# Performance work log

Hardware: AMD Instinct MI355X
Metric: run time of the kernel (lower is better)

## Reference

```python
import jax, jax.numpy as jnp
import numpy as np

EPS = 1e-5

def _bn(x):
    # training-mode batchnorm (batch stats), gamma=1 beta=0 per the module's init
    ax = tuple(range(x.ndim - 1))
    m = x.mean(ax, keepdims=True)
    v = x.var(ax, keepdims=True)
    return (x - m) * jax.lax.rsqrt(v + EPS)

def _mlp(x, weights):
    # shared 1x1-conv MLP: pointwise linear -> BN -> ReLU
    for W in weights:
        x = jax.nn.relu(_bn(jnp.einsum('...c,oc->...o', x, W)))
    return x

def _fps_single(xyz, npoint):
    # farthest point sampling, xyz [N,3] -> [npoint] int32 indices
    N = xyz.shape[0]
    def step(carry, _):
        dists, far = carry
        d = jnp.sum((xyz - xyz[far]) ** 2, -1)
        dists = jnp.minimum(dists, d)
        return (dists, jnp.argmax(dists).astype(jnp.int32)), far
    init = (jnp.full((N,), 1e10, xyz.dtype), jnp.int32(0))
    _, idx = jax.lax.scan(step, init, None, length=npoint)
    return idx

def _ball_query(new_xyz, xyz, radius, nsample):
    # first nsample points (in original order) within radius of each center
    d2 = jnp.sum((new_xyz[:, :, None, :] - xyz[:, None, :, :]) ** 2, -1)  # [B,S,N]
    N = xyz.shape[1]
    rank = jnp.where(d2 < radius * radius, jnp.arange(N, dtype=jnp.int32), jnp.int32(N))
    vals, _ = jax.lax.top_k(-rank, nsample)
    idx = -vals
    idx = jnp.where(idx == N, idx[..., :1], idx)  # pad with first valid (center itself)
    return idx

def _gather(pts, idx):
    # pts [B,N,C], idx [B,S,ns] -> [B,S,ns,C]
    B, S, ns = idx.shape
    return jnp.take_along_axis(pts, idx.reshape(B, S * ns, 1), axis=1).reshape(B, S, ns, pts.shape[-1])

def _sa(xyz, feats, npoint, radius, nsample, weights):
    fps_idx = jax.vmap(_fps_single, in_axes=(0, None))(xyz, npoint)
    new_xyz = jnp.take_along_axis(xyz, fps_idx[:, :, None], axis=1)  # [B,S,3]
    idx = _ball_query(new_xyz, xyz, radius, nsample)
    g_xyz = (_gather(xyz, idx) - new_xyz[:, :, None, :]) / radius  # normalize_xyz
    x = g_xyz if feats is None else jnp.concatenate([g_xyz, _gather(feats, idx)], -1)
    x = _mlp(x, weights)
    return new_xyz, x.max(axis=2), fps_idx  # maxpool over nsample

def _forward(obj_cloud, gripper_cloud, sa1_w0, sa1_w1, sa1_w2, sa2_w0, sa2_w1, sa2_w2,
             sa3_w0, sa3_w1, sa3_w2, ge_w0, ge_w1, ge_w2,
             head_w0, head_b0, head_w1, head_b1, head_w2, head_b2):
    # gripper encoder: pointwise conv1d MLP + global maxpool
    g = _mlp(gripper_cloud, [ge_w0, ge_w1, ge_w2])      # [B,G,128]
    gripper_feature = g.max(axis=1)                      # [B,128]
    # backbone
    xyz1, f1, _ = _sa(obj_cloud, None, 512, 0.2, 32, [sa1_w0, sa1_w1, sa1_w2])
    xyz2, f2, _ = _sa(xyz1, f1, 128, 0.4, 64, [sa2_w0, sa2_w1, sa2_w2])
    # sa3: group_all (use_xyz, no centering/normalization)
    x = jnp.concatenate([xyz2, f2], -1)[:, None]         # [B,1,128,259]
    x = _mlp(x, [sa3_w0, sa3_w1, sa3_w2])
    obj_feature = x.max(axis=2)[:, 0]                    # [B,1024]
    comb = jnp.concatenate([gripper_feature, obj_feature], -1)  # [B,1152]
    h = _bn(comb)
    h = jax.nn.relu(_bn(h @ head_w0.T + head_b0))
    h = jax.nn.relu(_bn(h @ head_w1.T + head_b1))
    return jax.nn.relu(h @ head_w2.T + head_b2)          # [B,1]

def setup_inputs() -> dict:
    key = jax.random.key(0)
    ks = jax.random.split(key, 24)
    def w(k, o, i):
        return (jax.random.normal(k, (o, i), jnp.float32) * 0.05)
    inp = {
        'obj_cloud': jax.random.uniform(ks[0], (8, 20000, 3), jnp.float32),
        'gripper_cloud': jax.random.uniform(ks[1], (8, 512, 3), jnp.float32),
        'sa1_w0': w(ks[2], 64, 3),   'sa1_w1': w(ks[3], 64, 64),   'sa1_w2': w(ks[4], 128, 64),
        'sa2_w0': w(ks[5], 128, 131),'sa2_w1': w(ks[6], 128, 128), 'sa2_w2': w(ks[7], 256, 128),
        'sa3_w0': w(ks[8], 256, 259),'sa3_w1': w(ks[9], 512, 256), 'sa3_w2': w(ks[10], 1024, 512),
        'ge_w0': w(ks[11], 64, 3),   'ge_w1': w(ks[12], 128, 64),  'ge_w2': w(ks[13], 128, 128),
        'head_w0': w(ks[14], 512, 1152), 'head_b0': jnp.zeros((512,), jnp.float32),
        'head_w1': w(ks[15], 256, 512),  'head_b1': jnp.zeros((256,), jnp.float32),
        'head_w2': w(ks[16], 1, 256),    'head_b2': jnp.zeros((1,), jnp.float32),
    }
    return inp

def reference(obj_cloud, gripper_cloud, sa1_w0, sa1_w1, sa1_w2, sa2_w0, sa2_w1, sa2_w2,
              sa3_w0, sa3_w1, sa3_w2, ge_w0, ge_w1, ge_w2,
              head_w0, head_b0, head_w1, head_b1, head_w2, head_b2):
    return _forward(obj_cloud, gripper_cloud, sa1_w0, sa1_w1, sa1_w2, sa2_w0, sa2_w1, sa2_w2,
                    sa3_w0, sa3_w1, sa3_w2, ge_w0, ge_w1, ge_w2,
                    head_w0, head_b0, head_w1, head_b1, head_w2, head_b2)
```

## Files before the change

### kernel.cpp

```cpp
#include <hip/hip_runtime.h>
#include <cstddef>
#include <cstdint>

#define EPS_BN 1e-5f
#define NBINS 4
#define NEG_INF (-__builtin_inff())

template <bool FUSE_IN, bool FUSE_MAX>
__global__ __launch_bounds__(256) void gemm_xwt(const float* __restrict__ X,
                                                const float* __restrict__ Wm,
                                                float* __restrict__ Y,
                                                int R, int Cin, int Cout,
                                                const float* __restrict__ st_in, int Rin,
                                                float* __restrict__ st_out,
                                                float* __restrict__ pooled, int ns) {
  __shared__ __align__(16) float Xs[16][132];
  __shared__ __align__(16) float Ws[16][132];
  __shared__ float sMean[512], sScale[512];
  const int t  = threadIdx.x;
  const int r0 = blockIdx.x << 7;
  const int n0 = blockIdx.y << 7;
  const int tx = t & 15;
  const int ty = t >> 4;

  if constexpr (FUSE_IN) {
    const float inv = 1.f / (float)Rin;
    for (int k = t; k < Cin; k += 256) {
      float s = 0.f, q = 0.f;
#pragma unroll
      for (int bn = 0; bn < NBINS; ++bn) {
        s += st_in[bn * 2 * Cin + k];
        q += st_in[bn * 2 * Cin + Cin + k];
      }
      const float m  = s * inv;
      const float vr = fmaf(-m, m, q * inv);
      sMean[k]  = m;
      sScale[k] = rsqrtf(vr + EPS_BN);
    }
    __syncthreads();
  }

  float acc[8][8] = {};
  const int rStage = t >> 1;
  const int kBase  = (t & 1) << 3;
  const int nr     = n0 + rStage;

  for (int k0 = 0; k0 < Cin; k0 += 16) {
    const float* xrow = X  + (size_t)(r0 + rStage) * Cin + k0 + kBase;
    const float* wrow = Wm + (size_t)nr * Cin + k0 + kBase;
    if (((Cin & 3) == 0) && (k0 + 16 <= Cin)) {
      float4 xa = *(const float4*)(xrow);
      float4 xb = *(const float4*)(xrow + 4);
      if constexpr (FUSE_IN) {
        const int kb = k0 + kBase;
        xa.x = fmaxf(0.f, (xa.x - sMean[kb + 0]) * sScale[kb + 0]);
        xa.y = fmaxf(0.f, (xa.y - sMean[kb + 1]) * sScale[kb + 1]);
        xa.z = fmaxf(0.f, (xa.z - sMean[kb + 2]) * sScale[kb + 2]);
        xa.w = fmaxf(0.f, (xa.w - sMean[kb + 3]) * sScale[kb + 3]);
        xb.x = fmaxf(0.f, (xb.x - sMean[kb + 4]) * sScale[kb + 4]);
        xb.y = fmaxf(0.f, (xb.y - sMean[kb + 5]) * sScale[kb + 5]);
        xb.z = fmaxf(0.f, (xb.z - sMean[kb + 6]) * sScale[kb + 6]);
        xb.w = fmaxf(0.f, (xb.w - sMean[kb + 7]) * sScale[kb + 7]);
      }
      Xs[kBase + 0][rStage] = xa.x; Xs[kBase + 1][rStage] = xa.y;
      Xs[kBase + 2][rStage] = xa.z; Xs[kBase + 3][rStage] = xa.w;
      Xs[kBase + 4][rStage] = xb.x; Xs[kBase + 5][rStage] = xb.y;
      Xs[kBase + 6][rStage] = xb.z; Xs[kBase + 7][rStage] = xb.w;
      float4 wa = {0, 0, 0, 0}, wb = {0, 0, 0, 0};
      if (nr < Cout) { wa = *(const float4*)(wrow); wb = *(const float4*)(wrow + 4); }
      Ws[kBase + 0][rStage] = wa.x; Ws[kBase + 1][rStage] = wa.y;
      Ws[kBase + 2][rStage] = wa.z; Ws[kBase + 3][rStage] = wa.w;
      Ws[kBase + 4][rStage] = wb.x; Ws[kBase + 5][rStage] = wb.y;
      Ws[kBase + 6][rStage] = wb.z; Ws[kBase + 7][rStage] = wb.w;
    } else {
#pragma unroll
      for (int u = 0; u < 8; ++u) {
        const int k = k0 + kBase + u;
        float xe = 0.f, we = 0.f;
        if (k < Cin) {
          xe = xrow[u];
          if constexpr (FUSE_IN) xe = fmaxf(0.f, (xe - sMean[k]) * sScale[k]);
          if (nr < Cout) we = wrow[u];
        }
        Xs[kBase + u][rStage] = xe;
        Ws[kBase + u][rStage] = we;
      }
    }
    __syncthreads();
#pragma unroll
    for (int kk = 0; kk < 16; ++kk) {
      const float4 a0 = *(const float4*)(&Xs[kk][ty << 2]);
      const float4 a1 = *(const float4*)(&Xs[kk][64 + (ty << 2)]);
      const float4 b0 = *(const float4*)(&Ws[kk][tx << 2]);
      const float4 b1 = *(const float4*)(&Ws[kk][64 + (tx << 2)]);
      const float av[8] = {a0.x, a0.y, a0.z, a0.w, a1.x, a1.y, a1.z, a1.w};
      const float bw[8] = {b0.x, b0.y, b0.z, b0.w, b1.x, b1.y, b1.z, b1.w};
#pragma unroll
      for (int i = 0; i < 8; ++i)
#pragma unroll
        for (int j = 0; j < 8; ++j) acc[i][j] = fmaf(av[i], bw[j], acc[i][j]);
    }
    __syncthreads();
  }
  if constexpr (!FUSE_MAX) {
#pragma unroll
    for (int h = 0; h < 2; ++h)
#pragma unroll
      for (int i = 0; i < 4; ++i) {
        const int r = r0 + h * 64 + (ty << 2) + i;
        float* yr = Y + (size_t)r * Cout;
#pragma unroll
        for (int g = 0; g < 2; ++g) {
          const int n = n0 + g * 64 + (tx << 2);
          if (n < Cout) {
            float4 o = {acc[h * 4 + i][g * 4 + 0], acc[h * 4 + i][g * 4 + 1],
                        acc[h * 4 + i][g * 4 + 2], acc[h * 4 + i][g * 4 + 3]};
            *(float4*)(yr + n) = o;
          }
        }
      }
  }
#pragma unroll
  for (int g = 0; g < 2; ++g)
#pragma unroll
    for (int j = 0; j < 4; ++j) {
      float s = 0.f, q = 0.f;
#pragma unroll
      for (int rh = 0; rh < 8; ++rh) {
        const float v = acc[rh][g * 4 + j];
        s += v;
        q = fmaf(v, v, q);
      }
      Xs[ty][g * 64 + (tx << 2) + j] = s;
      Ws[ty][g * 64 + (tx << 2) + j] = q;
    }
  __syncthreads();
  if (t < 128) {
    const int n = n0 + t;
    if (n < Cout) {
      float s = 0.f, q = 0.f;
#pragma unroll
      for (int w = 0; w < 16; ++w) { s += Xs[w][t]; q += Ws[w][t]; }
      float* dst = st_out + (blockIdx.x & (NBINS - 1)) * 2 * Cout;
      atomicAdd(dst + n, s);
      atomicAdd(dst + Cout + n, q);
    }
  }
  if constexpr (FUSE_MAX) {
    __syncthreads();
    float mxAll = NEG_INF;
#pragma unroll
    for (int h = 0; h < 2; ++h) {
#pragma unroll
      for (int g2 = 0; g2 < 2; ++g2)
#pragma unroll
        for (int j = 0; j < 4; ++j) {
          float mx = acc[h * 4 + 0][g2 * 4 + j];
          mx = fmaxf(mx, acc[h * 4 + 1][g2 * 4 + j]);
          mx = fmaxf(mx, acc[h * 4 + 2][g2 * 4 + j]);
          mx = fmaxf(mx, acc[h * 4 + 3][g2 * 4 + j]);
          Xs[ty][g2 * 64 + (tx << 2) + j] = mx;
        }
      __syncthreads();
      if (t < 128) {
        const int n = n0 + t;
        if (n < Cout) {
          if (ns <= 64) {
            const int tpg = ns >> 2;
            const int gph = 64 / ns;
            for (int gq = 0; gq < gph; ++gq) {
              float mx = NEG_INF;
              for (int w = gq * tpg; w < gq * tpg + tpg; ++w) mx = fmaxf(mx, Xs[w][t]);
              const int g = (r0 + h * 64) / ns + gq;
              pooled[(size_t)g * Cout + n] = mx;
            }
          } else {
            float mx = NEG_INF;
            for (int w = 0; w < 16; ++w) mx = fmaxf(mx, Xs[w][t]);
            mxAll = fmaxf(mxAll, mx);
          }
        }
      }
      __syncthreads();
    }
    if (ns > 64 && t < 128) {
      const int n = n0 + t;
      if (n < Cout) pooled[(size_t)(r0 >> 7) * Cout + n] = mxAll;
    }
  }
}

__global__ void bn_apply_pooled(const float* __restrict__ P, const float* __restrict__ st,
                                float* __restrict__ o, int G, int C, int Rtrue) {
  const int i = blockIdx.x * 256 + threadIdx.x;
  if (i >= G * C) return;
  const int c = i % C;
  float s = 0.f, q = 0.f;
#pragma unroll
  for (int bn = 0; bn < NBINS; ++bn) {
    s += st[bn * 2 * C + c];
    q += st[bn * 2 * C + C + c];
  }
  const float inv = 1.f / (float)Rtrue;
  const float m  = s * inv;
  const float vr = fmaf(-m, m, q * inv);
  const float sc = rsqrtf(vr + EPS_BN);
  o[i] = fmaxf(0.f, (P[i] - m) * sc);
}

__global__ void bn_apply_relu_maxpool(const float* __restrict__ Y,
                                      const float* __restrict__ st,
                                      float* __restrict__ o, int G, int ns, int C) {
  const int i = blockIdx.x * 256 + threadIdx.x;
  if (i >= G * C) return;
  const int c = i % C;
  const int g = i / C;
  float s = 0.f, q = 0.f;
#pragma unroll
  for (int bn = 0; bn < NBINS; ++bn) {
    s += st[bn * 2 * C + c];
    q += st[bn * 2 * C + C + c];
  }
  const int R = G * ns;
  const float inv = 1.f / (float)R;
  const float m  = s * inv;
  const float vr = fmaf(-m, m, q * inv);
  const float sc = rsqrtf(vr + EPS_BN);
  const float* p = Y + (size_t)g * ns * C + c;
  float mx = NEG_INF;
  for (int k = 0; k < ns; ++k) mx = fmaxf(mx, p[(size_t)k * C]);
  o[i] = fmaxf(0.f, (mx - m) * sc);
}

#define FPS_N 20000
#define FPS_S 512
#define FPS_NC 6
#define FPS_NCELL 216

__global__ __launch_bounds__(1024)
void fps_sa1_kernel(const float* __restrict__ xyz, float* __restrict__ new_xyz,
                    float* __restrict__ scratch) {
  const int b    = blockIdx.x;
  const int tid  = threadIdx.x;
  const int lane = tid & 63;
  const int wave = tid >> 6;
  const float* p = xyz + (size_t)b * FPS_N * 3;
  float* gxs = scratch + (size_t)b * FPS_N * 4;
  float* gys = gxs + FPS_N;
  float* gzs = gys + FPS_N;
  int*   gis = (int*)(gzs + FPS_N);

  __shared__ float ddS[FPS_N];
  __shared__ int   cStart[FPS_NCELL + 1];
  __shared__ int   cCnt[FPS_NCELL];
  __shared__ int   cFill[FPS_NCELL];
  __shared__ float ubV[FPS_NCELL];
  __shared__ int   ubI[FPS_NCELL];
  __shared__ float ubX[FPS_NCELL], ubY[FPS_NCELL], ubZ[FPS_NCELL];
  __shared__ float bc[3];
  __shared__ float wred[16 * 6];
  __shared__ float sC[10];

  float mnx = 1e30f, mny = 1e30f, mnz = 1e30f;
  float mxx = -1e30f, mxy = -1e30f, mxz = -1e30f;
  for (int i = tid; i < FPS_N; i += 1024) {
    const float x = p[i * 3 + 0], y = p[i * 3 + 1], z = p[i * 3 + 2];
    mnx = fminf(mnx, x); mny = fminf(mny, y); mnz = fminf(mnz, z);
    mxx = fmaxf(mxx, x); mxy = fmaxf(mxy, y); mxz = fmaxf(mxz, z);
  }
#pragma unroll
  for (int m = 1; m < 64; m <<= 1) {
    mnx = fminf(mnx, __shfl_xor(mnx, m, 64));
    mny = fminf(mny, __shfl_xor(mny, m, 64));
    mnz = fminf(mnz, __shfl_xor(mnz, m, 64));
    mxx = fmaxf(mxx, __shfl_xor(mxx, m, 64));
    mxy = fmaxf(mxy, __shfl_xor(mxy, m, 64));
    mxz = fmaxf(mxz, __shfl_xor(mxz, m, 64));
  }
  if (lane == 0) {
    wred[wave * 6 + 0] = mnx; wred[wave * 6 + 1] = mny; wred[wave * 6 + 2] = mnz;
    wred[wave * 6 + 3] = mxx; wred[wave * 6 + 4] = mxy; wred[wave * 6 + 5] = mxz;
  }
  if (tid < FPS_NCELL) { cCnt[tid] = 0; cFill[tid] = 0; }
  __syncthreads();
  if (tid == 0) {
    float a0 = wred[0], a1 = wred[1], a2 = wred[2];
    float a3 = wred[3], a4 = wred[4], a5 = wred[5];
    for (int w = 1; w < 16; ++w) {
      a0 = fminf(a0, wred[w * 6 + 0]); a1 = fminf(a1, wred[w * 6 + 1]);
      a2 = fminf(a2, wred[w * 6 + 2]); a3 = fmaxf(a3, wred[w * 6 + 3]);
      a4 = fmaxf(a4, wred[w * 6 + 4]); a5 = fmaxf(a5, wred[w * 6 + 5]);
    }
    const float ex = fmaxf(a3 - a0, 1e-9f);
    const float ey = fmaxf(a4 - a1, 1e-9f);
    const float ez = fmaxf(a5 - a2, 1e-9f);
    sC[0] = a0; sC[1] = a1; sC[2] = a2;
    sC[3] = (float)FPS_NC / ex; sC[4] = (float)FPS_NC / ey; sC[5] = (float)FPS_NC / ez;
    sC[6] = ex / (float)FPS_NC; sC[7] = ey / (float)FPS_NC; sC[8] = ez / (float)FPS_NC;
    sC[9] = fmaxf(ex, fmaxf(ey, ez)) * 1e-5f;
  }
  __syncthreads();
  const float bx0 = sC[0], by0 = sC[1], bz0 = sC[2];
  const float scx = sC[3], scy = sC[4], scz = sC[5];
  const float hx  = sC[6], hy  = sC[7], hz  = sC[8], ec = sC[9];

  for (int i = tid; i < FPS_N; i += 1024) {
    const float x = p[i * 3 + 0], y = p[i * 3 + 1], z = p[i * 3 + 2];
    const int cx = min(FPS_NC - 1, max(0, (int)((x - bx0) * scx)));
    const int cy = min(FPS_NC - 1, max(0, (int)((y - by0) * scy)));
    const int cz = min(FPS_NC - 1, max(0, (int)((z - bz0) * scz)));
    atomicAdd(&cCnt[(cx * FPS_NC + cy) * FPS_NC + cz], 1);
  }
  __syncthreads();
  if (tid == 0) {
    int acc = 0;
    for (int k = 0; k < FPS_NCELL; ++k) { cStart[k] = acc; acc += cCnt[k]; }
    cStart[FPS_NCELL] = acc;
  }
  __syncthreads();
  for (int i = tid; i < FPS_N; i += 1024) {
    const float x = p[i * 3 + 0], y = p[i * 3 + 1], z = p[i * 3 + 2];
    const int cx = min(FPS_NC - 1, max(0, (int)((x - bx0) * scx)));
    const int cy = min(FPS_NC - 1, max(0, (int)((y - by0) * scy)));
    const int cz = min(FPS_NC - 1, max(0, (int)((z - bz0) * scz)));
    const int cid = (cx * FPS_NC + cy) * FPS_NC + cz;
    const int pos = cStart[cid] + atomicAdd(&cFill[cid], 1);
    gxs[pos] = x; gys[pos] = y; gzs[pos] = z; gis[pos] = i;
  }
  for (int j = tid; j < FPS_N; j += 1024) ddS[j] = 1e10f;
  if (tid < FPS_NCELL) {
    ubV[tid] = (cCnt[tid] > 0) ? 1e10f : NEG_INF;
    ubI[tid] = 0x7fffffff;
  }
  __syncthreads();

  float fx = p[0], fy = p[1], fz = p[2];
  if (tid == 0) {
    float* o = new_xyz + (size_t)b * FPS_S * 3;
    o[0] = fx; o[1] = fy; o[2] = fz;
  }

  for (int s = 1; s < FPS_S; ++s) {
    const int cq = wave + (lane << 4);
    bool aff = false;
    if (cq < FPS_NCELL) {
      const int cx  = cq / (FPS_NC * FPS_NC);
      const int rem = cq - cx * (FPS_NC * FPS_NC);
      const int cy  = rem / FPS_NC;
      const int cz  = rem - cy * FPS_NC;
      const float lox = fmaf((float)cx, hx, bx0) - ec;
      const float hix = fmaf((float)(cx + 1), hx, bx0) + ec;
      const float loy = fmaf((float)cy, hy, by0) - ec;
      const float hiy = fmaf((float)(cy + 1), hy, by0) + ec;
      const float loz = fmaf((float)cz, hz, bz0) - ec;
      const float hiz = fmaf((float)(cz + 1), hz, bz0) + ec;
      const float dx = fmaxf(0.f, fmaxf(lox - fx, fx - hix));
      const float dy = fmaxf(0.f, fmaxf(loy - fy, fy - hiy));
      const float dz = fmaxf(0.f, fmaxf(loz - fz, fz - hiz));
      const float dmin = dx * dx + dy * dy + dz * dz;
      aff = (dmin * 0.99999f < ubV[cq]);
    }
    unsigned long long am = __ballot(aff);
    while (am) {
      const int l = __ffsll((long long)am) - 1;
      am &= am - 1;
      const int cc  = wave + (l << 4);
      const int st0 = cStart[cc];
      const int cn  = cStart[cc + 1] - st0;
      float bv = NEG_INF; int bi = 0x7fffffff;
      float bx = 0.f, by = 0.f, bz = 0.f;
      for (int j = lane; j < cn; j += 64) {
        const int g = st0 + j;
        const float qx = gxs[g], qy = gys[g], qz = gzs[g];
        const float dx = qx - fx, dy = qy - fy, dz = qz - fz;
        const float d  = __fadd_rn(__fadd_rn(__fmul_rn(dx, dx), __fmul_rn(dy, dy)),
                                   __fmul_rn(dz, dz));
        const float nd = fminf(ddS[g], d);
        ddS[g] = nd;
        const int gi = gis[g];
        if (nd > bv || (nd == bv && gi < bi)) { bv = nd; bi = gi; bx = qx; by = qy; bz = qz; }
      }
      float v = bv; int i0 = bi;
#pragma unroll
      for (int m = 1; m < 64; m <<= 1) {
        const float ov = __shfl_xor(v, m, 64);
        const int   oi = __shfl_xor(i0, m, 64);
        if (ov > v || (ov == v && oi < i0)) { v = ov; i0 = oi; }
      }
      if (v == bv && i0 == bi && bi != 0x7fffffff) {
        ubV[cc] = v; ubI[cc] = i0; ubX[cc] = bx; ubY[cc] = by; ubZ[cc] = bz;
      }
    }
    __syncthreads();
    if (tid < 64) {
      float v = NEG_INF; int i0 = 0x7fffffff; int c0 = 0;
#pragma unroll
      for (int q = 0; q < 4; ++q) {
        const int k = lane + (q << 6);
        if (k < FPS_NCELL) {
          const float ov = ubV[k]; const int oi = ubI[k];
          if (ov > v || (ov == v && oi < i0)) { v = ov; i0 = oi; c0 = k; }
        }
      }
#pragma unroll
      for (int m = 1; m < 64; m <<= 1) {
        const float ov = __shfl_xor(v, m, 64);
        const int   oi = __shfl_xor(i0, m, 64);
        const int   oc = __shfl_xor(c0, m, 64);
        if (ov > v || (ov == v && oi < i0)) { v = ov; i0 = oi; c0 = oc; }
      }
      if (lane == 0) {
        const float wx = ubX[c0], wy = ubY[c0], wz = ubZ[c0];
        bc[0] = wx; bc[1] = wy; bc[2] = wz;
        float* o = new_xyz + ((size_t)b * FPS_S + s) * 3;
        o[0] = wx; o[1] = wy; o[2] = wz;
      }
    }
    __syncthreads();
    fx = bc[0]; fy = bc[1]; fz = bc[2];
  }
}

template <int N, int NP, int THREADS, int NPT>
__global__ __launch_bounds__(THREADS)
void fps2_kernel(const float* __restrict__ xyz, float* __restrict__ new_xyz) {
  constexpr int NW = THREADS / 64;
  const int b    = blockIdx.x;
  const int tid  = threadIdx.x;
  const int lane = tid & 63;
  const int wave = tid >> 6;
  const float* p = xyz + (size_t)b * N * 3;
  float px[NPT], py[NPT], pz[NPT], dd[NPT];
#pragma unroll
  for (int j = 0; j < NPT; ++j) {
    const int i = tid + j * THREADS;
    if (i < N) {
      px[j] = p[i * 3 + 0];
      py[j] = p[i * 3 + 1];
      pz[j] = p[i * 3 + 2];
      dd[j] = 1e10f;
    } else {
      px[j] = 0.f; py[j] = 0.f; pz[j] = 0.f;
      dd[j] = NEG_INF;
    }
  }
  __shared__ float sv[NW], sx[NW], sy[NW], sz[NW];
  __shared__ int   si[NW];
  __shared__ float bc[3];
  float fx = p[0], fy = p[1], fz = p[2];
  if (tid == 0) {
    float* o = new_xyz + (size_t)b * NP * 3;
    o[0] = fx; o[1] = fy; o[2] = fz;
  }
  for (int s = 1; s < NP; ++s) {
    float bv = NEG_INF;
    int   bi = 0x7fffffff;
    float bx = 0.f, by = 0.f, bz = 0.f;
#pragma unroll
    for (int j = 0; j < NPT; ++j) {
      const float dx = px[j] - fx;
      const float dy = py[j] - fy;
      const float dz = pz[j] - fz;
      const float d  = __fadd_rn(__fadd_rn(__fmul_rn(dx, dx), __fmul_rn(dy, dy)),
                                 __fmul_rn(dz, dz));
      const float nd = fminf(dd[j], d);
      dd[j] = nd;
      if (nd > bv) { bv = nd; bi = tid + j * THREADS; bx = px[j]; by = py[j]; bz = pz[j]; }
    }
    float v = bv;
    int   i0 = bi;
#pragma unroll
    for (int m = 1; m < 64; m <<= 1) {
      const float ov = __shfl_xor(v, m, 64);
      const int   oi = __shfl_xor(i0, m, 64);
      if (ov > v || (ov == v && oi < i0)) { v = ov; i0 = oi; }
    }
    if (i0 == bi) {
      sv[wave] = bv; si[wave] = bi; sx[wave] = bx; sy[wave] = by; sz[wave] = bz;
    }
    __syncthreads();
    if (tid < 64) {
      const float lv = (lane < NW) ? sv[lane] : NEG_INF;
      const int   li = (lane < NW) ? si[lane] : 0x7fffffff;
      float v2 = lv;
      int   i2 = li;
#pragma unroll
      for (int m = 1; m < NW; m <<= 1) {
        const float ov = __shfl_xor(v2, m, 64);
        const int   oi = __shfl_xor(i2, m, 64);
        if (ov > v2 || (ov == v2 && oi < i2)) { v2 = ov; i2 = oi; }
      }
      if (lane < NW && li == i2) {
        const float wx = sx[lane], wy = sy[lane], wz = sz[lane];
        bc[0] = wx; bc[1] = wy; bc[2] = wz;
        float* o = new_xyz + ((size_t)b * NP + s) * 3;
        o[0] = wx; o[1] = wy; o[2] = wz;
      }
    }
    __syncthreads();
    fx = bc[0]; fy = bc[1]; fz = bc[2];
  }
}

template <int N, int NS>
__global__ __launch_bounds__(256)
void ballquery_wave_kernel(const float* __restrict__ centers,
                           const float* __restrict__ pts,
                           int* __restrict__ idx, int BS, int S, float r2) {
  const int w    = (blockIdx.x * 256 + threadIdx.x) >> 6;
  const int lane = threadIdx.x & 63;
  if (w >= BS) return;
  const int b = w / S;
  const float cx = centers[w * 3 + 0];
  const float cy = centers[w * 3 + 1];
  const float cz = centers[w * 3 + 2];
  const float* p = pts + (size_t)b * N * 3;
  int* o = idx + (size_t)w * NS;
  int total = 0;
  int first = -1;
  for (int i0 = 0; i0 < N && total < NS; i0 += 64) {
    const int i = i0 + lane;
    bool pred = false;
    if (i < N) {
      const float dx = cx - p[i * 3 + 0];
      const float dy = cy - p[i * 3 + 1];
      const float dz = cz - p[i * 3 + 2];
      const float d2 = __fadd_rn(__fadd_rn(__fmul_rn(dx, dx), __fmul_rn(dy, dy)),
                                 __fmul_rn(dz, dz));
      pred = (d2 < r2);
    }
    const unsigned long long mask = __ballot(pred);
    if (mask) {
      const unsigned long long below = (lane == 0) ? 0ull : (mask << (64 - lane));
      const int before = __popcll(below);
      if (pred && (total + before) < NS) o[total + before] = i;
      if (first < 0) first = i0 + (__ffsll((long long)mask) - 1);
      total += __popcll(mask);
    }
  }
  if (lane >= total && lane < NS) o[lane] = first;
}

__global__ void group1_kernel(const float* __restrict__ xyz, const float* __restrict__ ctr,
                              const int* __restrict__ idx, float* __restrict__ X1) {
  const int t = blockIdx.x * 256 + threadIdx.x;
  if (t >= 8 * 512 * 32) return;
  const int g = t >> 5;
  const int b = g >> 9;
  const int i = idx[t];
  const float* p = xyz + ((size_t)b * 20000 + i) * 3;
  const float* c = ctr + (size_t)g * 3;
  X1[t * 3 + 0] = (p[0] - c[0]) / 0.2f;
  X1[t * 3 + 1] = (p[1] - c[1]) / 0.2f;
  X1[t * 3 + 2] = (p[2] - c[2]) / 0.2f;
}

__global__ void group2_kernel(const float* __restrict__ xyz1,
                              const float* __restrict__ xyz2,
                              const float* __restrict__ f1,
                              const int* __restrict__ idx2,
                              float* __restrict__ X2) {
  const int t = blockIdx.x * 256 + threadIdx.x;
  if (t >= 65536 * 131) return;
  const int r = t / 131;
  const int c = t - r * 131;
  const int g = r >> 6;
  const int b = g >> 7;
  const int i = idx2[r];
  float v;
  if (c < 3) {
    v = (xyz1[((size_t)b * 512 + i) * 3 + c] - xyz2[(size_t)g * 3 + c]) / 0.4f;
  } else {
    v = f1[((size_t)b * 512 + i) * 128 + (c - 3)];
  }
  X2[t] = v;
}

__global__ void build_x3_kernel(const float* __restrict__ xyz2, const float* __restrict__ f2,
                                float* __restrict__ X3) {
  const int t = blockIdx.x * 256 + threadIdx.x;
  if (t >= 1024 * 259) return;
  const int r = t / 259;
  const int c = t - r * 259;
  X3[t] = (c < 3) ? xyz2[r * 3 + c] : f2[(size_t)r * 256 + (c - 3)];
}

__global__ __launch_bounds__(512) void head_kernel(
    const float* __restrict__ gfeat, const float* __restrict__ objf,
    const float* __restrict__ w0, const float* __restrict__ b0,
    const float* __restrict__ w1, const float* __restrict__ b1,
    const float* __restrict__ w2, const float* __restrict__ b2,
    float* __restrict__ out) {
  __shared__ __align__(16) float comb[8 * 1152];
  __shared__ __align__(16) float h1[8 * 512];
  __shared__ __align__(16) float h2[8 * 256];
  const int tid = threadIdx.x;
  for (int i = tid; i < 8 * 1152; i += 512) {
    const int b = i / 1152, c = i - b * 1152;
    comb[i] = (c < 128) ? gfeat[b * 128 + c] : objf[b * 1024 + (c - 128)];
  }
  __syncthreads();
  for (int c = tid; c < 1152; c += 512) {
    float s = 0.f;
#pragma unroll
    for (int b = 0; b < 8; ++b) s += comb[b * 1152 + c];
    const float m = s * 0.125f;
    float v = 0.f;
#pragma unroll
    for (int b = 0; b < 8; ++b) { const float d = comb[b * 1152 + c] - m; v = fmaf(d, d, v); }
    const float sc = rsqrtf(v * 0.125f + EPS_BN);
#pragma unroll
    for (int b = 0; b < 8; ++b) comb[b * 1152 + c] = (comb[b * 1152 + c] - m) * sc;
  }
  __syncthreads();
  {
    float a[8];
#pragma unroll
    for (int b = 0; b < 8; ++b) a[b] = b0[tid];
    const float* wr = w0 + (size_t)tid * 1152;
    for (int ci = 0; ci < 1152; ci += 4) {
      const float4 wv = *(const float4*)(wr + ci);
#pragma unroll
      for (int b = 0; b < 8; ++b) {
        const float4 xv = *(const float4*)(&comb[b * 1152 + ci]);
        a[b] = fmaf(xv.x, wv.x, a[b]);
        a[b] = fmaf(xv.y, wv.y, a[b]);
        a[b] = fmaf(xv.z, wv.z, a[b]);
        a[b] = fmaf(xv.w, wv.w, a[b]);
      }
    }
    float s = 0.f;
#pragma unroll
    for (int b = 0; b < 8; ++b) s += a[b];
    const float m = s * 0.125f;
    float v = 0.f;
#pragma unroll
    for (int b = 0; b < 8; ++b) { const float d = a[b] - m; v = fmaf(d, d, v); }
    const float sc = rsqrtf(v * 0.125f + EPS_BN);
#pragma unroll
    for (int b = 0; b < 8; ++b) h1[b * 512 + tid] = fmaxf(0.f, (a[b] - m) * sc);
  }
  __syncthreads();
  if (tid < 256) {
    float a[8];
#pragma unroll
    for (int b = 0; b < 8; ++b) a[b] = b1[tid];
    const float* wr = w1 + (size_t)tid * 512;
    for (int ci = 0; ci < 512; ci += 4) {
      const float4 wv = *(const float4*)(wr + ci);
#pragma unroll
      for (int b = 0; b < 8; ++b) {
        const float4 xv = *(const float4*)(&h1[b * 512 + ci]);
        a[b] = fmaf(xv.x, wv.x, a[b]);
        a[b] = fmaf(xv.y, wv.y, a[b]);
        a[b] = fmaf(xv.z, wv.z, a[b]);
        a[b] = fmaf(xv.w, wv.w, a[b]);
      }
    }
    float s = 0.f;
#pragma unroll
    for (int b = 0; b < 8; ++b) s += a[b];
    const float m = s * 0.125f;
    float v = 0.f;
#pragma unroll
    for (int b = 0; b < 8; ++b) { const float d = a[b] - m; v = fmaf(d, d, v); }
    const float sc = rsqrtf(v * 0.125f + EPS_BN);
#pragma unroll
    for (int b = 0; b < 8; ++b) h2[b * 256 + tid] = fmaxf(0.f, (a[b] - m) * sc);
  }
  __syncthreads();
  if (tid < 8) {
    float s = b2[0];
    for (int ci = 0; ci < 256; ++ci) s = fmaf(h2[tid * 256 + ci], w2[ci], s);
    out[tid] = fmaxf(0.f, s);
  }
}

extern "C" void kernel_launch(void* const* d_in, const int* in_sizes, int n_in,
                              void* d_out, int out_size, void* d_ws, size_t ws_size,
                              hipStream_t stream) {
  (void)in_sizes; (void)n_in; (void)out_size; (void)ws_size;
  const float* obj  = (const float*)d_in[0];
  const float* grip = (const float*)d_in[1];
  const float* s1w0 = (const float*)d_in[2];
  const float* s1w1 = (const float*)d_in[3];
  const float* s1w2 = (const float*)d_in[4];
  const float* s2w0 = (const float*)d_in[5];
  const float* s2w1 = (const float*)d_in[6];
  const float* s2w2 = (const float*)d_in[7];
  const float* s3w0 = (const float*)d_in[8];
  const float* s3w1 = (const float*)d_in[9];
  const float* s3w2 = (const float*)d_in[10];
  const float* gw0  = (const float*)d_in[11];
  const float* gw1  = (const float*)d_in[12];
  const float* gw2  = (const float*)d_in[13];
  const float* hw0  = (const float*)d_in[14];
  const float* hb0  = (const float*)d_in[15];
  const float* hw1  = (const float*)d_in[16];
  const float* hb1  = (const float*)d_in[17];
  const float* hw2  = (const float*)d_in[18];
  const float* hb2  = (const float*)d_in[19];
  float* out = (float*)d_out;

  float* wsf   = (float*)d_ws;
  float* stats = wsf;
  float* xyz1  = wsf + 23040;
  float* xyz2  = wsf + 35328;
  float* gfeat = wsf + 38400;
  float* objf  = wsf + 39424;
  float* f1    = wsf + 47616;
  float* f2    = wsf + 571904;
  float* x3    = wsf + 834048;
  int*   idx1  = (int*)(wsf + 1099264);
  int*   idx2  = (int*)(wsf + 1230336);
  float* bufP  = wsf + 1295872;
  float* bufQ  = wsf + 18073088;
  float* fpsScratch = bufP + 8388608;

  static const int st_off[12] = {0, 512, 1536, 2560, 3072, 3584,
                                 4608, 5632, 6656, 8704, 10752, 14848};
  auto st = [&](int li) { return stats + st_off[li]; };

  hipMemsetAsync(stats, 0, 23040 * sizeof(float), stream);

  auto gemm0 = [&](const float* X, const float* Wm, float* Y, int R, int Cin, int Cout,
                   int lo) {
    dim3 g((R + 127) / 128, (Cout + 127) / 128);
    gemm_xwt<false, false><<<g, 256, 0, stream>>>(X, Wm, Y, R, Cin, Cout, nullptr, 0,
                                                  st(lo), nullptr, 0);
  };
  auto gemmf = [&](const float* X, const float* Wm, float* Y, int R, int Cin, int Cout,
                   int li, int lo) {
    dim3 g((R + 127) / 128, (Cout + 127) / 128);
    gemm_xwt<true, false><<<g, 256, 0, stream>>>(X, Wm, Y, R, Cin, Cout, st(li), R,
                                                 st(lo), nullptr, 0);
  };
  auto gemmfM = [&](const float* X, const float* Wm, float* pooled, int R, int Cin,
                    int Cout, int li, int lo, int ns) {
    dim3 g((R + 127) / 128, (Cout + 127) / 128);
    gemm_xwt<true, true><<<g, 256, 0, stream>>>(X, Wm, nullptr, R, Cin, Cout, st(li), R,
                                                st(lo), pooled, ns);
  };
  auto applymax_k = [&](const float* Y, int li, int G, int ns, int C, float* o) {
    const int n = G * C;
    bn_apply_relu_maxpool<<<(n + 255) / 256, 256, 0, stream>>>(Y, st(li), o, G, ns, C);
  };
  auto applypool_k = [&](const float* P, int li, int G, int C, int Rtrue, float* o) {
    const int n = G * C;
    bn_apply_pooled<<<(n + 255) / 256, 256, 0, stream>>>(P, st(li), o, G, C, Rtrue);
  };

  fps_sa1_kernel<<<8, 1024, 0, stream>>>(obj, xyz1, fpsScratch);

  float* gY1 = bufP;
  float* gY2 = bufP + 262144;
  float* gY3 = bufP + 786432;
  gemm0(grip, gw0, gY1, 4096, 3, 64, 0);
  gemmf(gY1, gw1, gY2, 4096, 64, 128, 0, 1);
  gemmf(gY2, gw2, gY3, 4096, 128, 128, 1, 2);
  applymax_k(gY3, 2, 8, 512, 128, gfeat);

  ballquery_wave_kernel<20000, 32><<<1024, 256, 0, stream>>>(xyz1, obj, idx1, 4096, 512, 0.04f);
  float* X1 = bufQ;
  group1_kernel<<<512, 256, 0, stream>>>(obj, xyz1, idx1, X1);
  gemm0(X1, s1w0, bufP, 131072, 3, 64, 3);
  gemmf(bufP, s1w1, bufQ, 131072, 64, 64, 3, 4);
  gemmfM(bufQ, s1w2, bufP, 131072, 64, 128, 4, 5, 32);
  applypool_k(bufP, 5, 4096, 128, 131072, f1);

  fps2_kernel<512, 128, 256, 2><<<8, 256, 0, stream>>>(xyz1, xyz2);
  ballquery_wave_kernel<512, 64><<<256, 256, 0, stream>>>(xyz2, xyz1, idx2, 1024, 128, 0.16f);
  float* X2 = bufQ;
  group2_kernel<<<(65536 * 131 + 255) / 256, 256, 0, stream>>>(xyz1, xyz2, f1, idx2, X2);
  gemm0(X2, s2w0, bufP, 65536, 131, 128, 6);
  gemmf(bufP, s2w1, bufQ, 65536, 128, 128, 6, 7);
  gemmfM(bufQ, s2w2, bufP, 65536, 128, 256, 7, 8, 64);
  applypool_k(bufP, 8, 1024, 256, 65536, f2);

  build_x3_kernel<<<(1024 * 259 + 255) / 256, 256, 0, stream>>>(xyz2, f2, x3);
  float* Y3a = bufQ;
  float* Y3b = bufQ + 262144;
  float* Y3p = bufQ + 786432;
  gemm0(x3, s3w0, Y3a, 1024, 259, 256, 9);
  gemmf(Y3a, s3w1, Y3b, 1024, 256, 512, 9, 10);
  gemmfM(Y3b, s3w2, Y3p, 1024, 512, 1024, 10, 11, 128);
  applypool_k(Y3p, 11, 8, 1024, 1024, objf);

  head_kernel<<<1, 512, 0, stream>>>(gfeat, objf, hw0, hb0, hw1, hb1, hw2, hb2, out);
}
```

Before: 2.662 ms.

## Process FPS cells with 16-lane groups, precompute cell bounds, pack points as float4

In the SA1 farthest-point-sampling kernel, each affected grid cell is now scanned by a 16-lane subgroup instead of a whole 64-lane wave. This lets four cells be processed per wave at once and shortens the reductions to 16-lane shuffles. Cell bounding boxes are precomputed once into shared memory instead of being recomputed every iteration. Sorted points are stored as a single float4 (xyz plus the index bit-cast into w) so each point is one vector load. The risk is lane imbalance: large cells are walked by only 16 lanes, and divergence grows when few cells are affected per step.

```diff
diff --git a/kernel.cpp b/kernel.cpp
--- a/kernel.cpp
+++ b/kernel.cpp
@@ -244,11 +244,10 @@
   const int tid  = threadIdx.x;
   const int lane = tid & 63;
   const int wave = tid >> 6;
+  const int lg   = lane & 15;
+  const int grp  = tid >> 4;
   const float* p = xyz + (size_t)b * FPS_N * 3;
-  float* gxs = scratch + (size_t)b * FPS_N * 4;
-  float* gys = gxs + FPS_N;
-  float* gzs = gys + FPS_N;
-  int*   gis = (int*)(gzs + FPS_N);
+  float4* g4 = (float4*)(scratch + (size_t)b * FPS_N * 4);
 
   __shared__ float ddS[FPS_N];
   __shared__ int   cStart[FPS_NCELL + 1];
@@ -257,6 +256,8 @@
   __shared__ float ubV[FPS_NCELL];
   __shared__ int   ubI[FPS_NCELL];
   __shared__ float ubX[FPS_NCELL], ubY[FPS_NCELL], ubZ[FPS_NCELL];
+  __shared__ float cLoX[FPS_NCELL], cLoY[FPS_NCELL], cLoZ[FPS_NCELL];
+  __shared__ float cHiX[FPS_NCELL], cHiY[FPS_NCELL], cHiZ[FPS_NCELL];
   __shared__ float bc[3];
   __shared__ float wred[16 * 6];
   __shared__ float sC[10];
@@ -311,6 +312,18 @@
     const int cz = min(FPS_NC - 1, max(0, (int)((z - bz0) * scz)));
     atomicAdd(&cCnt[(cx * FPS_NC + cy) * FPS_NC + cz], 1);
   }
+  if (tid < FPS_NCELL) {
+    const int cx  = tid / (FPS_NC * FPS_NC);
+    const int rem = tid - cx * (FPS_NC * FPS_NC);
+    const int cy  = rem / FPS_NC;
+    const int cz  = rem - cy * FPS_NC;
+    cLoX[tid] = fmaf((float)cx, hx, bx0) - ec;
+    cHiX[tid] = fmaf((float)(cx + 1), hx, bx0) + ec;
+    cLoY[tid] = fmaf((float)cy, hy, by0) - ec;
+    cHiY[tid] = fmaf((float)(cy + 1), hy, by0) + ec;
+    cLoZ[tid] = fmaf((float)cz, hz, bz0) - ec;
+    cHiZ[tid] = fmaf((float)(cz + 1), hz, bz0) + ec;
+  }
   __syncthreads();
   if (tid == 0) {
     int acc = 0;
@@ -325,7 +338,8 @@
     const int cz = min(FPS_NC - 1, max(0, (int)((z - bz0) * scz)));
     const int cid = (cx * FPS_NC + cy) * FPS_NC + cz;
     const int pos = cStart[cid] + atomicAdd(&cFill[cid], 1);
-    gxs[pos] = x; gys[pos] = y; gzs[pos] = z; gis[pos] = i;
+    float4 v4; v4.x = x; v4.y = y; v4.z = z; v4.w = __int_as_float(i);
+    g4[pos] = v4;
   }
   for (int j = tid; j < FPS_N; j += 1024) ddS[j] = 1e10f;
   if (tid < FPS_NCELL) {
@@ -341,54 +355,44 @@
   }
 
   for (int s = 1; s < FPS_S; ++s) {
-    const int cq = wave + (lane << 4);
-    bool aff = false;
-    if (cq < FPS_NCELL) {
-      const int cx  = cq / (FPS_NC * FPS_NC);
-      const int rem = cq - cx * (FPS_NC * FPS_NC);
-      const int cy  = rem / FPS_NC;
-      const int cz  = rem - cy * FPS_NC;
-      const float lox = fmaf((float)cx, hx, bx0) - ec;
-      const float hix = fmaf((float)(cx + 1), hx, bx0) + ec;
-      const float loy = fmaf((float)cy, hy, by0) - ec;
-      const float hiy = fmaf((float)(cy + 1), hy, by0) + ec;
-      const float loz = fmaf((float)cz, hz, bz0) - ec;
-      const float hiz = fmaf((float)(cz + 1), hz, bz0) + ec;
-      const float dx = fmaxf(0.f, fmaxf(lox - fx, fx - hix));
-      const float dy = fmaxf(0.f, fmaxf(loy - fy, fy - hiy));
-      const float dz = fmaxf(0.f, fmaxf(loz - fz, fz - hiz));
-      const float dmin = dx * dx + dy * dy + dz * dz;
-      aff = (dmin * 0.99999f < ubV[cq]);
-    }
-    unsigned long long am = __ballot(aff);
-    while (am) {
-      const int l = __ffsll((long long)am) - 1;
-      am &= am - 1;
-      const int cc  = wave + (l << 4);
-      const int st0 = cStart[cc];
-      const int cn  = cStart[cc + 1] - st0;
+#pragma unroll
+    for (int q = 0; q < 4; ++q) {
+      const int cid = grp + (q << 6);
+      bool aff = false;
+      if (cid < FPS_NCELL) {
+        const float dx = fmaxf(0.f, fmaxf(cLoX[cid] - fx, fx - cHiX[cid]));
+        const float dy = fmaxf(0.f, fmaxf(cLoY[cid] - fy, fy - cHiY[cid]));
+        const float dz = fmaxf(0.f, fmaxf(cLoZ[cid] - fz, fz - cHiZ[cid]));
+        const float dmin = dx * dx + dy * dy + dz * dz;
+        aff = (dmin * 0.99999f < ubV[cid]);
+      }
+      if (__ballot(aff) == 0ull) continue;
       float bv = NEG_INF; int bi = 0x7fffffff;
       float bx = 0.f, by = 0.f, bz = 0.f;
-      for (int j = lane; j < cn; j += 64) {
-        const int g = st0 + j;
-        const float qx = gxs[g], qy = gys[g], qz = gzs[g];
-        const float dx = qx - fx, dy = qy - fy, dz = qz - fz;
-        const float d  = __fadd_rn(__fadd_rn(__fmul_rn(dx, dx), __fmul_rn(dy, dy)),
-                                   __fmul_rn(dz, dz));
-        const float nd = fminf(ddS[g], d);
-        ddS[g] = nd;
-        const int gi = gis[g];
-        if (nd > bv || (nd == bv && gi < bi)) { bv = nd; bi = gi; bx = qx; by = qy; bz = qz; }
+      if (aff) {
+        const int st0 = cStart[cid];
+        const int cn  = cStart[cid + 1] - st0;
+        for (int j = lg; j < cn; j += 16) {
+          const int g = st0 + j;
+          const float4 q4 = g4[g];
+          const float dx = q4.x - fx, dy = q4.y - fy, dz = q4.z - fz;
+          const float d  = __fadd_rn(__fadd_rn(__fmul_rn(dx, dx), __fmul_rn(dy, dy)),
+                                     __fmul_rn(dz, dz));
+          const float nd = fminf(ddS[g], d);
+          ddS[g] = nd;
+          const int gi = __float_as_int(q4.w);
+          if (nd > bv || (nd == bv && gi < bi)) { bv = nd; bi = gi; bx = q4.x; by = q4.y; bz = q4.z; }
+        }
       }
       float v = bv; int i0 = bi;
 #pragma unroll
-      for (int m = 1; m < 64; m <<= 1) {
-        const float ov = __shfl_xor(v, m, 64);
-        const int   oi = __shfl_xor(i0, m, 64);
+      for (int m = 1; m < 16; m <<= 1) {
+        const float ov = __shfl_xor(v, m, 16);
+        const int   oi = __shfl_xor(i0, m, 16);
         if (ov > v || (ov == v && oi < i0)) { v = ov; i0 = oi; }
       }
-      if (v == bv && i0 == bi && bi != 0x7fffffff) {
-        ubV[cc] = v; ubI[cc] = i0; ubX[cc] = bx; ubY[cc] = by; ubZ[cc] = bz;
+      if (aff && i0 == bi && bi != 0x7fffffff) {
+        ubV[cid] = v; ubI[cid] = i0; ubX[cid] = bx; ubY[cid] = by; ubZ[cid] = bz;
       }
     }
     __syncthreads();
```

Measured after the change: 2.919 ms. 1.1x slower.
